# Kernel optimization log

Hardware: AMD Instinct MI355X
Metric: run time of the kernel (lower is better)

## Reference

```python
import jax, jax.numpy as jnp
import numpy as np

B, N, H, W = 1, 256, 32, 32
C_LIDAR, C_RGB, K, S = 64, 64, 16, 3
MLP3 = [128, 64, 64]


def _l2norm(x, eps=1e-12):
    n = jnp.linalg.norm(x, axis=-1, keepdims=True)
    return x / jnp.maximum(n, eps)


def _cal_sim(src, dst):
    # src [B,N,C], dst [B,M,C] -> [B,N,M,2] (cosine sim normalized two ways)
    s = _l2norm(src)
    d = _l2norm(dst)
    sim = jnp.einsum('bmc,bnc->bmn', d, s)  # [B,M,N]
    dst_src = sim / (jnp.max(sim, axis=2, keepdims=True) + 1e-10)
    src_dst = jnp.swapaxes(sim, 1, 2)       # [B,N,M]
    src_dst = src_dst / (jnp.max(src_dst, axis=2, keepdims=True) + 1e-6)
    return jnp.stack([src_dst, jnp.swapaxes(dst_src, 1, 2)], axis=-1)


def _mlp(x, layers):
    # 1x1 conv + (identity-init BN folded) + ReLU chain, channel-last
    for w, b in layers:
        x = jax.nn.relu(x @ w + b)
    return x


def _unfold(x, s):
    # F.unfold with zero pad s//2: [B,C,H,W] -> [B, H*W, s*s, C]
    p = s // 2
    b, c, h, w = x.shape
    xp = jnp.pad(x, ((0, 0), (0, 0), (p, p), (p, p)))
    pats = jnp.stack([xp[:, :, i:i + h, j:j + w] for i in range(s) for j in range(s)], axis=2)
    return pats.reshape(b, c, s * s, h * w).transpose(0, 3, 2, 1)


def _weighted_pnp(src_xyz, uv, wgt):
    # weighted SVD (Kabsch) head: lift uv to 3D at source depth, solve R,t
    z = src_xyz[..., 2:3]
    dst = jnp.concatenate([uv, jnp.ones_like(z)], axis=-1) * z
    wn = wgt / (jnp.sum(wgt, axis=-1, keepdims=True) + 1e-8)
    sc = jnp.einsum('bn,bnc->bc', wn, src_xyz)
    dc = jnp.einsum('bn,bnc->bc', wn, dst)
    s_c = src_xyz - sc[:, None]
    d_c = dst - dc[:, None]
    Hm = jnp.einsum('bn,bni,bnj->bij', wn, s_c, d_c)
    U, _, Vt = jnp.linalg.svd(Hm)
    V = jnp.swapaxes(Vt, -1, -2)
    det = jnp.linalg.det(jnp.einsum('bik,bjk->bij', V, U))
    diag = jnp.stack([jnp.ones_like(det), jnp.ones_like(det), det], axis=-1)
    R = jnp.einsum('bik,bk,bjk->bij', V, diag, U)
    t = dc - jnp.einsum('bij,bj->bi', R, sc)
    return R, t


def reference(warped_xyz, warped_points, RF3, RF3_index, lidar_z,
              w2_0, b2_0, w2_1, b2_1, w2_2, b2_2,
              w3_0, b3_0, w3_1, b3_1, w3_2, b3_2,
              w1_0, b1_0, w1_1, b1_1, w1_2, b1_2,
              wm_0, bm_0, wm_1, bm_1, wm_2, bm_2):
    b, n, _ = warped_xyz.shape
    _, ci, h, w = RF3.shape
    m = h * w
    xyz = warped_xyz * lidar_z                       # [B,N,3]
    rf = RF3.transpose(0, 2, 3, 1).reshape(b, m, ci)   # [B,M,Ci]
    rfi = RF3_index.transpose(0, 2, 3, 1).reshape(b, m, 3)

    src_dst_sim = _cal_sim(warped_points, rf)        # [B,N,M,2]

    # kNN grouping of the point cloud onto itself
    d2 = jnp.sum((xyz[:, :, None, :] - xyz[:, None, :, :]) ** 2, axis=-1)
    _, idx = jax.lax.top_k(-d2, K)                   # [B,N,K]
    gather = jax.vmap(lambda pts, i: pts[i])
    pc_xyz_g = gather(xyz, idx)                      # [B,N,K,3]
    pc_pts_g = gather(warped_points, idx)            # [B,N,K,C]
    diff = pc_xyz_g - xyz[:, :, None, :]
    dn = jnp.linalg.norm(diff, axis=-1, keepdims=True)
    pc_nbr = jnp.concatenate([pc_pts_g, diff, dn], axis=-1)
    wts = _mlp(pc_nbr, [(w2_0, b2_0), (w2_1, b2_1), (w2_2, b2_2)])
    wts = jnp.max(wts, axis=-1, keepdims=True)
    wts = jax.nn.softmax(wts, axis=-2)
    pc_feats = jnp.sum(wts * pc_pts_g, axis=-2)      # [B,N,C]

    # image 3x3 neighbor grouping via unfold
    rf_nbr_idx = _unfold(RF3_index, S)               # [B,M,SS,3]
    rf_nbr_pts = _unfold(RF3, S)                     # [B,M,SS,Ci]
    iw = _mlp(jnp.concatenate([rf_nbr_idx, rf_nbr_pts], axis=-1),
              [(w3_0, b3_0), (w3_1, b3_1), (w3_2, b3_2)])
    iw = jnp.max(iw, axis=-1, keepdims=True)
    iw = jax.nn.softmax(iw, axis=-2)
    img_feats = jnp.sum(iw * rf_nbr_pts, axis=-2)    # [B,M,Ci]

    nbr_sim = _cal_sim(pc_feats, img_feats)          # [B,N,M,2]

    feats = jnp.concatenate([
        jnp.broadcast_to(xyz[:, :, None, :], (b, n, m, 3)),
        jnp.broadcast_to(rfi[:, None, :, :], (b, n, m, 3)),
        jnp.broadcast_to(warped_points[:, :, None, :], (b, n, m, warped_points.shape[-1])),
        jnp.broadcast_to(rf[:, None, :, :], (b, n, m, ci)),
        src_dst_sim, nbr_sim], axis=-1)              # [B,N,M,6+C+Ci+4]
    feats = _mlp(feats, [(w1_0, b1_0), (w1_1, b1_1), (w1_2, b1_2)])

    aw = jax.nn.softmax(jnp.max(feats, axis=-1), axis=-1)   # [B,N,M]
    corres_uv1 = jnp.einsum('bnm,bmc->bnc', aw, rfi)         # [B,N,3]
    att = jnp.einsum('bnm,bnmc->bnc', aw, feats)             # [B,N,64]
    att = _mlp(att, [(wm_0, bm_0), (wm_1, bm_1)])
    logits = att @ wm_2 + bm_2                               # [B,N,2]
    weights = jax.nn.softmax(logits, axis=-1)
    w_in = jnp.argmax(weights, axis=-1).astype(weights.dtype)
    R, t = _weighted_pnp(xyz, corres_uv1[..., :2], w_in)
    return R, t, weights


def setup_inputs():
    key = jax.random.key(0)
    ks = jax.random.split(key, 32)
    f32 = jnp.float32
    inp = {}
    inp['warped_xyz'] = jax.random.normal(ks[0], (B, N, 3), f32)
    inp['warped_points'] = jax.random.normal(ks[1], (B, N, C_LIDAR), f32)
    inp['RF3'] = jax.random.normal(ks[2], (B, C_RGB, H, W), f32)
    inp['RF3_index'] = jax.random.normal(ks[3], (B, 3, H, W), f32)
    inp['lidar_z'] = jax.random.uniform(ks[4], (B, N, 1), f32, 0.5, 2.0)
    wdims = {'w2_0': (4 + C_LIDAR, C_LIDAR), 'w2_1': (C_LIDAR, C_LIDAR), 'w2_2': (C_LIDAR, C_LIDAR),
             'w3_0': (3 + C_RGB, C_RGB), 'w3_1': (C_RGB, C_RGB), 'w3_2': (C_RGB, C_RGB),
             'w1_0': (6 + C_RGB + C_LIDAR + 4, MLP3[0]), 'w1_1': (MLP3[0], MLP3[1]), 'w1_2': (MLP3[1], MLP3[2]),
             'wm_0': (MLP3[2], MLP3[2]), 'wm_1': (MLP3[2], MLP3[0]), 'wm_2': (MLP3[0], 2)}
    for i, (name, d) in enumerate(wdims.items()):
        inp[name] = jax.random.normal(ks[5 + i], d, f32) * 0.05
        inp['b' + name[1:]] = jnp.zeros((d[1],), f32)
    return inp
```

## Files before the change

kernel.cpp:

```cpp
#include <hip/hip_runtime.h>
#include <math.h>


typedef _Float16 f16;
typedef __attribute__((ext_vector_type(4))) _Float16 f16x4;
typedef __attribute__((ext_vector_type(8))) _Float16 f16x8;
typedef __attribute__((ext_vector_type(4))) float f32x4;

constexpr int WS_XYZ  = 0;
constexpr int WS_RF   = 768;
constexpr int WS_RFI  = WS_RF   + 65536;
constexpr int WS_SN   = WS_RFI  + 3072;
constexpr int WS_DN   = WS_SN   + 16384;
constexpr int WS_SIM1 = WS_DN   + 65536;
constexpr int WS_RM1  = WS_SIM1 + 262144;
constexpr int WS_CM1  = WS_RM1  + 1024;
constexpr int WS_PCF  = WS_CM1  + 256;
constexpr int WS_IMGF = WS_PCF  + 16384;
constexpr int WS_PCN  = WS_IMGF + 65536;
constexpr int WS_IMGN = WS_PCN  + 16384;
constexpr int WS_SIM2 = WS_IMGN + 65536;
constexpr int WS_RM2  = WS_SIM2 + 262144;
constexpr int WS_CM2  = WS_RM2  + 1024;
constexpr int WS_B1   = WS_CM2  + 256;
constexpr int WS_B2   = WS_B1   + 32768;
constexpr int WS_ATT  = WS_B2   + 131072;
constexpr int WS_UV   = WS_ATT  + 16384;
constexpr int WS_WIN  = WS_UV   + 768;
constexpr int WS_KNN  = WS_WIN  + 256;
constexpr int WS_PM   = WS_KNN  + 4096;
constexpr int WS_PS   = WS_PM   + 2048;
constexpr int WS_PATT = WS_PS   + 2048;
constexpr int WS_PUV  = WS_PATT + 131072;
constexpr int WS_W11T = WS_PUV  + 6144;
constexpr int WS_W12T = WS_W11T + 4096;
constexpr int WS_G3   = WS_W12T + 2048;
constexpr int WS_SIMF = WS_G3   + 65600;

__global__ __launch_bounds__(256) void prep_kernel(float* ws, const float* wxyz,
                                                   const float* lz, const float* RF3,
                                                   const float* RFI, const float* w11,
                                                   const float* w12) {
    int i = blockIdx.x * 256 + threadIdx.x;
    if (i < 768) {
        int n = i / 3;
        ws[WS_XYZ + i] = wxyz[i] * lz[n];
    } else if (i < 768 + 65536) {
        int j = i - 768; int mm = j >> 6, c = j & 63;
        ws[WS_RF + j] = RF3[c * 1024 + mm];
    } else if (i < 768 + 65536 + 3072) {
        int j = i - (768 + 65536); int mm = j / 3, c = j - mm * 3;
        ws[WS_RFI + j] = RFI[c * 1024 + mm];
    } else if (i < 69376 + 8192) {
        int j = i - 69376; int col = j >> 7, k = j & 127;
        ((f16*)(ws + WS_W11T))[col * 128 + k] = (f16)w11[k * 64 + col];
    } else if (i < 69376 + 12288) {
        int j = i - (69376 + 8192); int col = j >> 6, k = j & 63;
        ((f16*)(ws + WS_W12T))[col * 64 + k] = (f16)w12[k * 64 + col];
    }
}

__global__ __launch_bounds__(64) void rownorm2_kernel(const float* sA, float* dA,
                                                      const float* sB, float* dB) {
    int b = blockIdx.x, t = threadIdx.x;
    const float* src; float* dst; int r;
    if (b < 256) { src = sA; dst = dA; r = b; }
    else         { src = sB; dst = dB; r = b - 256; }
    float v = src[r * 64 + t];
    float s = v * v;
    for (int o = 32; o > 0; o >>= 1) s += __shfl_down(s, o);
    s = __shfl(s, 0);
    float nrm = sqrtf(s);
    dst[r * 64 + t] = v / fmaxf(nrm, 1e-12f);
}

__global__ __launch_bounds__(256) void sim_kernel(const float* dn, const float* sn,
                                                  float* sim, float* rmax) {
    __shared__ __align__(16) float dv[64];
    __shared__ float red[256];
    int m = blockIdx.x, t = threadIdx.x;
    if (t < 64) dv[t] = dn[m * 64 + t];
    __syncthreads();
    float acc = 0.f;
    const float4* sp = (const float4*)(sn + t * 64);
    const float4* dp = (const float4*)dv;
    for (int i = 0; i < 16; i++) {
        float4 s4 = sp[i], d4 = dp[i];
        acc += s4.x * d4.x + s4.y * d4.y + s4.z * d4.z + s4.w * d4.w;
    }
    sim[m * 256 + t] = acc;
    red[t] = acc; __syncthreads();
    for (int s = 128; s > 0; s >>= 1) {
        if (t < s) red[t] = fmaxf(red[t], red[t + s]);
        __syncthreads();
    }
    if (t == 0) rmax[m] = red[0];
}

__global__ __launch_bounds__(256) void simfeat_kernel(float* ws) {
    __shared__ float red[256];
    int n = blockIdx.x, t = threadIdx.x;
    const float* sim1 = ws + WS_SIM1;  const float* rm1g = ws + WS_RM1;
    const float* sim2 = ws + WS_SIM2;  const float* rm2g = ws + WS_RM2;
    f16* simfg = (f16*)(ws + WS_SIMF);
    float s1v[4], s2v[4];
    float mx1 = -INFINITY, mx2 = -INFINITY;
    for (int j = 0; j < 4; j++) {
        int m = t + j * 256;
        s1v[j] = sim1[m * 256 + n]; mx1 = fmaxf(mx1, s1v[j]);
        s2v[j] = sim2[m * 256 + n]; mx2 = fmaxf(mx2, s2v[j]);
    }
    red[t] = mx1; __syncthreads();
    for (int s = 128; s > 0; s >>= 1) {
        if (t < s) red[t] = fmaxf(red[t], red[t + s]);
        __syncthreads();
    }
    float cm1 = red[0];
    __syncthreads();
    red[t] = mx2; __syncthreads();
    for (int s = 128; s > 0; s >>= 1) {
        if (t < s) red[t] = fmaxf(red[t], red[t + s]);
        __syncthreads();
    }
    float cm2 = red[0];
    for (int j = 0; j < 4; j++) {
        int m = t + j * 256;
        float r1 = rm1g[m], r2 = rm2g[m];
        float f0 = s1v[j] / (cm1 + 1e-6f);
        float f1 = s1v[j] / (r1 + 1e-10f);
        float f2 = s2v[j] / (cm2 + 1e-6f);
        float f3 = s2v[j] / (r2 + 1e-10f);
        *(f16x4*)&simfg[(n * 1024 + m) * 4] =
            (f16x4){(f16)f0, (f16)f1, (f16)f2, (f16)f3};
    }
}

__global__ __launch_bounds__(256) void knn_kernel(float* ws) {
    const float* xyz = ws + WS_XYZ;
    int* knn = (int*)(ws + WS_KNN);
    __shared__ float px[256], py[256], pz[256], d2[256];
    __shared__ float rv[256];
    __shared__ int   ri[256];
    int n = blockIdx.x, t = threadIdx.x;
    px[t] = xyz[t * 3 + 0]; py[t] = xyz[t * 3 + 1]; pz[t] = xyz[t * 3 + 2];
    __syncthreads();
    float dx = px[t] - px[n], dy = py[t] - py[n], dz = pz[t] - pz[n];
    d2[t] = dx * dx + dy * dy + dz * dz;
    __syncthreads();
    for (int k = 0; k < 16; k++) {
        rv[t] = d2[t]; ri[t] = t;
        __syncthreads();
        for (int s = 128; s > 0; s >>= 1) {
            if (t < s) {
                float v2 = rv[t + s]; int i2 = ri[t + s];
                if (v2 < rv[t] || (v2 == rv[t] && i2 < ri[t])) { rv[t] = v2; ri[t] = i2; }
            }
            __syncthreads();
        }
        if (t == 0) { knn[n * 16 + k] = ri[0]; d2[ri[0]] = INFINITY; }
        __syncthreads();
    }
}

__global__ __launch_bounds__(256) void mlp2_kernel(float* ws, const float* wpts,
        const float* w0, const float* b0, const float* w1, const float* b1,
        const float* w2, const float* b2) {
    __shared__ float x[16 * 68], hA[16 * 68], hB[16 * 68];
    __shared__ int   kn[16];
    __shared__ float wv[16], wts[16];
    int n = blockIdx.x, t = threadIdx.x;
    const float* xyz = ws + WS_XYZ;
    const int* knn = (const int*)(ws + WS_KNN);
    if (t < 16) kn[t] = knn[n * 16 + t];
    __syncthreads();
    for (int i = t; i < 1024; i += 256) {
        int k = i >> 6, c = i & 63;
        x[k * 68 + c] = wpts[kn[k] * 64 + c];
    }
    if (t < 16) {
        int i = kn[t];
        float dx = xyz[i * 3 + 0] - xyz[n * 3 + 0];
        float dy = xyz[i * 3 + 1] - xyz[n * 3 + 1];
        float dz = xyz[i * 3 + 2] - xyz[n * 3 + 2];
        x[t * 68 + 64] = dx; x[t * 68 + 65] = dy; x[t * 68 + 66] = dz;
        x[t * 68 + 67] = sqrtf(dx * dx + dy * dy + dz * dz);
    }
    __syncthreads();
    for (int o = t; o < 1024; o += 256) {
        int k = o >> 6, j = o & 63; float acc = b0[j];
        for (int i = 0; i < 68; i++) acc += x[k * 68 + i] * w0[i * 64 + j];
        hA[k * 68 + j] = fmaxf(acc, 0.f);
    }
    __syncthreads();
    for (int o = t; o < 1024; o += 256) {
        int k = o >> 6, j = o & 63; float acc = b1[j];
        for (int i = 0; i < 64; i++) acc += hA[k * 68 + i] * w1[i * 64 + j];
        hB[k * 68 + j] = fmaxf(acc, 0.f);
    }
    __syncthreads();
    for (int o = t; o < 1024; o += 256) {
        int k = o >> 6, j = o & 63; float acc = b2[j];
        for (int i = 0; i < 64; i++) acc += hB[k * 68 + i] * w2[i * 64 + j];
        hA[k * 68 + j] = fmaxf(acc, 0.f);
    }
    __syncthreads();
    if (t < 16) {
        float mx = -INFINITY;
        for (int j = 0; j < 64; j++) mx = fmaxf(mx, hA[t * 68 + j]);
        wv[t] = mx;
    }
    __syncthreads();
    if (t < 16) {
        float mx = -INFINITY;
        for (int k = 0; k < 16; k++) mx = fmaxf(mx, wv[k]);
        float sum = 0.f;
        for (int k = 0; k < 16; k++) sum += expf(wv[k] - mx);
        wts[t] = expf(wv[t] - mx) / sum;
    }
    __syncthreads();
    if (t < 64) {
        float acc = 0.f;
        for (int k = 0; k < 16; k++) acc += wts[k] * x[k * 68 + t];
        ws[WS_PCF + n * 64 + t] = acc;
    }
}

__global__ __launch_bounds__(64) void g3_kernel(float* ws, const float* w0, const float* b0) {
    int m = blockIdx.x, j = threadIdx.x;
    float acc = b0[j];
    if (m < 1024) {
        for (int i = 0; i < 3; i++)  acc += ws[WS_RFI + m * 3 + i] * w0[i * 64 + j];
        for (int c = 0; c < 64; c++) acc += ws[WS_RF + m * 64 + c] * w0[(3 + c) * 64 + j];
    }
    ws[WS_G3 + m * 64 + j] = fmaxf(acc, 0.f);
}

__global__ __launch_bounds__(256) void mlp3_kernel(float* ws,
        const float* w1, const float* b1, const float* w2, const float* b2) {
    __shared__ float x1[36 * 68], h2[36 * 68];
    __shared__ float h3v[36], iw9[36];
    int m0 = blockIdx.x * 4, t = threadIdx.x;
    const float* G = ws + WS_G3;
    const float* rf = ws + WS_RF;
    for (int i = t; i < 36 * 64; i += 256) {
        int row = i >> 6, c = i & 63;
        int mi = row / 9, kk = row - mi * 9;
        int m = m0 + mi; int y = m >> 5, x = m & 31;
        int dy = kk / 3 - 1, dx = kk % 3 - 1;
        int ny = y + dy, nx = x + dx;
        bool val = (ny >= 0 && ny < 32 && nx >= 0 && nx < 32);
        int idx = val ? (ny * 32 + nx) : 1024;
        x1[row * 68 + c] = G[idx * 64 + c];
    }
    __syncthreads();
    for (int o = t; o < 36 * 64; o += 256) {
        int row = o >> 6, c = o & 63; float acc = b1[c];
        for (int i = 0; i < 64; i++) acc += x1[row * 68 + i] * w1[i * 64 + c];
        h2[row * 68 + c] = fmaxf(acc, 0.f);
    }
    __syncthreads();
    for (int o = t; o < 36 * 64; o += 256) {
        int row = o >> 6, c = o & 63; float acc = b2[c];
        for (int i = 0; i < 64; i++) acc += h2[row * 68 + i] * w2[i * 64 + c];
        x1[row * 68 + c] = fmaxf(acc, 0.f);
    }
    __syncthreads();
    if (t < 36) {
        float mx = -INFINITY;
        for (int c = 0; c < 64; c++) mx = fmaxf(mx, x1[t * 68 + c]);
        h3v[t] = mx;
    }
    __syncthreads();
    if (t < 36) {
        int mi = t / 9;
        float mx = -INFINITY;
        for (int k = 0; k < 9; k++) mx = fmaxf(mx, h3v[mi * 9 + k]);
        float sum = 0.f;
        for (int k = 0; k < 9; k++) sum += expf(h3v[mi * 9 + k] - mx);
        iw9[t] = expf(h3v[t] - mx) / sum;
    }
    __syncthreads();
    {
        int mi = t >> 6, c = t & 63;
        int m = m0 + mi; int y = m >> 5, x = m & 31;
        float acc = 0.f;
        for (int kk = 0; kk < 9; kk++) {
            int dy = kk / 3 - 1, dx = kk % 3 - 1;
            int ny = y + dy, nx = x + dx;
            bool val = (ny >= 0 && ny < 32 && nx >= 0 && nx < 32);
            if (val) acc += iw9[mi * 9 + kk] * rf[(ny * 32 + nx) * 64 + c];
        }
        ws[WS_IMGF + m * 64 + c] = acc;
    }
}

__global__ __launch_bounds__(128) void base12_kernel(float* ws, const float* wpts,
                                                     const float* w10, const float* b10) {
    int b = blockIdx.x, j = threadIdx.x;
    if (b < 256) {
        int n = b;
        float acc = b10[j];
        for (int i = 0; i < 3; i++)  acc += ws[WS_XYZ + n * 3 + i] * w10[i * 128 + j];
        for (int c = 0; c < 64; c++) acc += wpts[n * 64 + c] * w10[(6 + c) * 128 + j];
        ws[WS_B1 + n * 128 + j] = acc;
    } else {
        int m = b - 256;
        float acc = 0.f;
        for (int i = 0; i < 3; i++)  acc += ws[WS_RFI + m * 3 + i] * w10[(3 + i) * 128 + j];
        for (int c = 0; c < 64; c++) acc += ws[WS_RF + m * 64 + c] * w10[(70 + c) * 128 + j];
        ws[WS_B2 + m * 128 + j] = acc;
    }
}

__global__ __launch_bounds__(256) void mlp1_kernel(float* ws, const float* w10,
        const float* b11, const float* b12) {
    __shared__ __align__(16) f16 H1h[64 * 136];
    __shared__ __align__(16) f16 H2h[64 * 72];
    __shared__ float base1n[128];
    __shared__ float simw[4 * 128];
    __shared__ float rmPart[4][64];
    int n = blockIdx.y, seg = blockIdx.x, t = threadIdx.x;
    int wave = t >> 6, lane = t & 63, q = lane >> 4, l16 = lane & 15;
    int col = wave * 16 + l16;
    const float* base2 = ws + WS_B2;
    const float* rfig = ws + WS_RFI;
    const f16* simfg = (const f16*)(ws + WS_SIMF);
    const f16* w11t = (const f16*)(ws + WS_W11T);
    const f16* w12t = (const f16*)(ws + WS_W12T);
    if (t < 128) base1n[t] = ws[WS_B1 + n * 128 + t];
    for (int i = t; i < 512; i += 256) simw[i] = w10[134 * 128 + i];
    f16x8 B2f[4], B3f[2];
    for (int s = 0; s < 4; s++) B2f[s] = *(const f16x8*)&w11t[col * 128 + s * 32 + q * 8];
    for (int s = 0; s < 2; s++) B3f[s] = *(const f16x8*)&w12t[col * 64 + s * 32 + q * 8];
    float bias2 = b11[col], bias3 = b12[col];
    float attAcc = 0.f;
    float uv0 = 0.f, uv1 = 0.f, uv2 = 0.f;
    float Mv = -INFINITY, Sv = 0.f;
    int mBeg = seg * 128;
    __syncthreads();
    for (int c4 = 0; c4 < 2; c4++) {
        int m0 = mBeg + c4 * 64;
        for (int idx = t; idx < 2048; idx += 256) {
            int row = idx >> 5, k4 = (idx & 31) * 4;
            int m = m0 + row;
            f16x4 sf = *(const f16x4*)&simfg[(n * 1024 + m) * 4];
            float s0 = (float)sf[0], s1 = (float)sf[1], s2 = (float)sf[2], s3 = (float)sf[3];
            float4 bs = *(const float4*)&base2[m * 128 + k4];
            float4 b1v = *(const float4*)&base1n[k4];
            float4 w0v = *(const float4*)&simw[k4];
            float4 w1v = *(const float4*)&simw[128 + k4];
            float4 w2v = *(const float4*)&simw[256 + k4];
            float4 w3v = *(const float4*)&simw[384 + k4];
            float v0 = b1v.x + bs.x + s0 * w0v.x + s1 * w1v.x + s2 * w2v.x + s3 * w3v.x;
            float v1 = b1v.y + bs.y + s0 * w0v.y + s1 * w1v.y + s2 * w2v.y + s3 * w3v.y;
            float v2 = b1v.z + bs.z + s0 * w0v.z + s1 * w1v.z + s2 * w2v.z + s3 * w3v.z;
            float v3 = b1v.w + bs.w + s0 * w0v.w + s1 * w1v.w + s2 * w2v.w + s3 * w3v.w;
            *(f16x4*)&H1h[row * 136 + k4] = (f16x4){
                (f16)fmaxf(v0, 0.f), (f16)fmaxf(v1, 0.f),
                (f16)fmaxf(v2, 0.f), (f16)fmaxf(v3, 0.f)};
        }
        __syncthreads();
        f32x4 a[4];
        for (int tl = 0; tl < 4; tl++) a[tl] = (f32x4){bias2, bias2, bias2, bias2};
        for (int s = 0; s < 4; s++)
            for (int tl = 0; tl < 4; tl++) {
                f16x8 f = *(const f16x8*)&H1h[(tl * 16 + l16) * 136 + s * 32 + q * 8];
                a[tl] = __builtin_amdgcn_mfma_f32_16x16x32_f16(f, B2f[s], a[tl], 0, 0, 0);
            }
        for (int tl = 0; tl < 4; tl++)
            for (int r = 0; r < 4; r++)
                H2h[(tl * 16 + q * 4 + r) * 72 + col] = (f16)fmaxf(a[tl][r], 0.f);
        __syncthreads();
        f32x4 c3[4];
        for (int tl = 0; tl < 4; tl++) c3[tl] = (f32x4){bias3, bias3, bias3, bias3};
        for (int s = 0; s < 2; s++)
            for (int tl = 0; tl < 4; tl++) {
                f16x8 f = *(const f16x8*)&H2h[(tl * 16 + l16) * 72 + s * 32 + q * 8];
                c3[tl] = __builtin_amdgcn_mfma_f32_16x16x32_f16(f, B3f[s], c3[tl], 0, 0, 0);
            }
        for (int tl = 0; tl < 4; tl++)
            for (int r = 0; r < 4; r++)
                c3[tl][r] = fmaxf(c3[tl][r], 0.f);
        for (int tl = 0; tl < 4; tl++)
            for (int r = 0; r < 4; r++) {
                float v = c3[tl][r];
                v = fmaxf(v, __shfl_xor(v, 1));
                v = fmaxf(v, __shfl_xor(v, 2));
                v = fmaxf(v, __shfl_xor(v, 4));
                v = fmaxf(v, __shfl_xor(v, 8));
                if (l16 == 0) rmPart[wave][tl * 16 + q * 4 + r] = v;
            }
        __syncthreads();
        float rmv = fmaxf(fmaxf(rmPart[0][lane], rmPart[1][lane]),
// ... 102 lines not shown
        const int PQ[3][2] = {{0, 1}, {0, 2}, {1, 2}};
        for (int pp = 0; pp < 3; pp++) {
            int p = PQ[pp][0], q = PQ[pp][1];
            double apq = A[p][q];
            if (fabs(apq) < 1e-300) continue;
            double tau = (A[q][q] - A[p][p]) / (2.0 * apq);
            double tt = (tau >= 0.0 ? 1.0 : -1.0) / (fabs(tau) + sqrt(1.0 + tau * tau));
            double c = 1.0 / sqrt(1.0 + tt * tt), s = tt * c;
            for (int k = 0; k < 3; k++) {
                double akp = A[k][p], akq = A[k][q];
                A[k][p] = c * akp - s * akq; A[k][q] = s * akp + c * akq;
            }
            for (int k = 0; k < 3; k++) {
                double apk = A[p][k], aqk = A[q][k];
                A[p][k] = c * apk - s * aqk; A[q][k] = s * apk + c * aqk;
            }
            for (int k = 0; k < 3; k++) {
                double vkp = V[k][p], vkq = V[k][q];
                V[k][p] = c * vkp - s * vkq; V[k][q] = s * vkp + c * vkq;
            }
        }
    }
    double lam[3] = {A[0][0], A[1][1], A[2][2]};
    int o0 = 0, o1 = 1, o2 = 2;
    if (lam[o0] < lam[o1]) { int tp = o0; o0 = o1; o1 = tp; }
    if (lam[o0] < lam[o2]) { int tp = o0; o0 = o2; o2 = tp; }
    if (lam[o1] < lam[o2]) { int tp = o1; o1 = o2; o2 = tp; }
    int ord[3] = {o0, o1, o2};
    double v[3][3], u[3][3], R[3][3];
    for (int k = 0; k < 3; k++)
        for (int i = 0; i < 3; i++) v[k][i] = V[i][ord[k]];
    double sv0 = sqrt(fmax(lam[o0], 0.0));
    if (!(sv0 > 1e-150)) {
        for (int i = 0; i < 3; i++)
            for (int j = 0; j < 3; j++) R[i][j] = (i == j) ? 1.0 : 0.0;
    } else {
        double nn[3];
        for (int k = 0; k < 3; k++) {
            for (int i = 0; i < 3; i++)
                u[k][i] = Hd[i][0] * v[k][0] + Hd[i][1] * v[k][1] + Hd[i][2] * v[k][2];
            nn[k] = sqrt(u[k][0] * u[k][0] + u[k][1] * u[k][1] + u[k][2] * u[k][2]);
        }
        for (int i = 0; i < 3; i++) u[0][i] /= nn[0];
        if (nn[1] > 1e-12 * nn[0]) {
            for (int i = 0; i < 3; i++) u[1][i] /= nn[1];
        } else {
            int e = (fabs(u[0][0]) <= fabs(u[0][1]) && fabs(u[0][0]) <= fabs(u[0][2])) ? 0
                    : ((fabs(u[0][1]) <= fabs(u[0][2])) ? 1 : 2);
            double ev[3] = {0, 0, 0}; ev[e] = 1.0;
            double d0 = ev[0] * u[0][0] + ev[1] * u[0][1] + ev[2] * u[0][2];
            double w1v[3], wn2 = 0;
            for (int i = 0; i < 3; i++) { w1v[i] = ev[i] - d0 * u[0][i]; wn2 += w1v[i] * w1v[i]; }
            wn2 = sqrt(wn2);
            for (int i = 0; i < 3; i++) u[1][i] = w1v[i] / wn2;
        }
        if (nn[2] > 1e-10 * nn[0]) {
            for (int i = 0; i < 3; i++) u[2][i] /= nn[2];
        } else {
            u[2][0] = u[0][1] * u[1][2] - u[0][2] * u[1][1];
            u[2][1] = u[0][2] * u[1][0] - u[0][0] * u[1][2];
            u[2][2] = u[0][0] * u[1][1] - u[0][1] * u[1][0];
        }
        double cr[3] = {u[1][1] * u[2][2] - u[1][2] * u[2][1],
                        u[1][2] * u[2][0] - u[1][0] * u[2][2],
                        u[1][0] * u[2][1] - u[1][1] * u[2][0]};
        double detU = u[0][0] * cr[0] + u[0][1] * cr[1] + u[0][2] * cr[2];
        double cv[3] = {v[1][1] * v[2][2] - v[1][2] * v[2][1],
                        v[1][2] * v[2][0] - v[1][0] * v[2][2],
                        v[1][0] * v[2][1] - v[1][1] * v[2][0]};
        double detV = v[0][0] * cv[0] + v[0][1] * cv[1] + v[0][2] * cv[2];
        double dsign = detU * detV;
        for (int i = 0; i < 3; i++)
            for (int j = 0; j < 3; j++)
                R[i][j] = v[0][i] * u[0][j] + v[1][i] * u[1][j] + dsign * v[2][i] * u[2][j];
    }
    for (int i = 0; i < 3; i++) {
        double ti = dc[i] - (R[i][0] * sc[0] + R[i][1] * sc[1] + R[i][2] * sc[2]);
        out[9 + i] = (float)ti;
        for (int j = 0; j < 3; j++) out[i * 3 + j] = (float)R[i][j];
    }
}

__global__ __launch_bounds__(256) void pnp_kernel(float* ws, float* out) {
    __shared__ double red[256];
    int t = threadIdx.x;
    double w = (double)ws[WS_WIN + t];
    double x0 = ws[WS_XYZ + t * 3 + 0];
    double x1 = ws[WS_XYZ + t * 3 + 1];
    double x2 = ws[WS_XYZ + t * 3 + 2];
    double z = x2;
    double dd0 = (double)ws[WS_UV + t * 3 + 0] * z;
    double dd1 = (double)ws[WS_UV + t * 3 + 1] * z;
    double dd2 = z;
    auto reduce = [&](double v) -> double {
        red[t] = v; __syncthreads();
        for (int s = 128; s > 0; s >>= 1) {
            if (t < s) red[t] += red[t + s];
            __syncthreads();
        }
        double r = red[0]; __syncthreads();
        return r;
    };
    double wsum = reduce(w);
    double sx0 = reduce(w * x0), sx1 = reduce(w * x1), sx2 = reduce(w * x2);
    double sd0 = reduce(w * dd0), sd1 = reduce(w * dd1), sd2 = reduce(w * dd2);
    double inv = 1.0 / (wsum + 1e-8);
    double sc[3] = {sx0 * inv, sx1 * inv, sx2 * inv};
    double dc[3] = {sd0 * inv, sd1 * inv, sd2 * inv};
    double wn = w * inv;
    double a0 = x0 - sc[0], a1 = x1 - sc[1], a2 = x2 - sc[2];
    double b0 = dd0 - dc[0], b1 = dd1 - dc[1], b2 = dd2 - dc[2];
    double Hm[9];
    Hm[0] = reduce(wn * a0 * b0); Hm[1] = reduce(wn * a0 * b1); Hm[2] = reduce(wn * a0 * b2);
    Hm[3] = reduce(wn * a1 * b0); Hm[4] = reduce(wn * a1 * b1); Hm[5] = reduce(wn * a1 * b2);
    Hm[6] = reduce(wn * a2 * b0); Hm[7] = reduce(wn * a2 * b1); Hm[8] = reduce(wn * a2 * b2);
    if (t == 0) compute_rt(Hm, sc, dc, out);
}

extern "C" void kernel_launch(void* const* d_in, const int* in_sizes, int n_in,
                              void* d_out, int out_size, void* d_ws, size_t ws_size,
                              hipStream_t stream) {
    float* ws = (float*)d_ws;
    const float* wxyz = (const float*)d_in[0];
    const float* wpts = (const float*)d_in[1];
    const float* RF3  = (const float*)d_in[2];
    const float* RFI  = (const float*)d_in[3];
    const float* lz   = (const float*)d_in[4];
    const float* w2_0 = (const float*)d_in[5];  const float* b2_0 = (const float*)d_in[6];
    const float* w2_1 = (const float*)d_in[7];  const float* b2_1 = (const float*)d_in[8];
    const float* w2_2 = (const float*)d_in[9];  const float* b2_2 = (const float*)d_in[10];
    const float* w3_0 = (const float*)d_in[11]; const float* b3_0 = (const float*)d_in[12];
    const float* w3_1 = (const float*)d_in[13]; const float* b3_1 = (const float*)d_in[14];
    const float* w3_2 = (const float*)d_in[15]; const float* b3_2 = (const float*)d_in[16];
    const float* w1_0 = (const float*)d_in[17]; const float* b1_0 = (const float*)d_in[18];
    const float* w1_1 = (const float*)d_in[19]; const float* b1_1 = (const float*)d_in[20];
    const float* w1_2 = (const float*)d_in[21]; const float* b1_2 = (const float*)d_in[22];
    const float* wm_0 = (const float*)d_in[23]; const float* bm_0 = (const float*)d_in[24];
    const float* wm_1 = (const float*)d_in[25]; const float* bm_1 = (const float*)d_in[26];
    const float* wm_2 = (const float*)d_in[27]; const float* bm_2 = (const float*)d_in[28];
    float* out = (float*)d_out;

    prep_kernel<<<319, 256, 0, stream>>>(ws, wxyz, lz, RF3, RFI, w1_1, w1_2);
    rownorm2_kernel<<<1280, 64, 0, stream>>>(wpts, ws + WS_SN, ws + WS_RF, ws + WS_DN);
    sim_kernel<<<1024, 256, 0, stream>>>(ws + WS_DN, ws + WS_SN, ws + WS_SIM1, ws + WS_RM1);
    knn_kernel<<<256, 256, 0, stream>>>(ws);
    mlp2_kernel<<<256, 256, 0, stream>>>(ws, wpts, w2_0, b2_0, w2_1, b2_1, w2_2, b2_2);
    g3_kernel<<<1025, 64, 0, stream>>>(ws, w3_0, b3_0);
    mlp3_kernel<<<256, 256, 0, stream>>>(ws, w3_1, b3_1, w3_2, b3_2);
    rownorm2_kernel<<<1280, 64, 0, stream>>>(ws + WS_PCF, ws + WS_PCN, ws + WS_IMGF, ws + WS_IMGN);
    sim_kernel<<<1024, 256, 0, stream>>>(ws + WS_IMGN, ws + WS_PCN, ws + WS_SIM2, ws + WS_RM2);
    simfeat_kernel<<<256, 256, 0, stream>>>(ws);
    base12_kernel<<<1280, 128, 0, stream>>>(ws, wpts, w1_0, b1_0);
    mlp1_kernel<<<dim3(8, 256), 256, 0, stream>>>(ws, w1_0, b1_1, b1_2);
    combinehead_kernel<<<256, 128, 0, stream>>>(ws, wm_0, bm_0, wm_1, bm_1, wm_2, bm_2, out);
    pnp_kernel<<<1, 256, 0, stream>>>(ws, out);
}
```

Before: 262.8 us.

## Fuse pipeline stages to cut kernel launches and fold normalization into producers

Reduces the launch count from 14 to 9 kernels. Independent stages (g3, base12 and knn; mlp2 and mlp3) are merged into multi-role kernels selected by block index. The row L2 normalization is folded into sim1 as reciprocal-norm scaling and into the mlp2/mlp3 epilogues, which removes the rownorm passes. Max reductions now use wave shuffles, and the pnp reductions are batched so fewer barrier rounds run. The risks are block-role divergence and higher shared memory per block in the merged kernels.

```diff
diff --git a/kernel.cpp b/kernel.cpp
--- a/kernel.cpp
+++ b/kernel.cpp
@@ -11,6 +11,8 @@
 constexpr int WS_RF   = 768;
 constexpr int WS_RFI  = WS_RF   + 65536;
 constexpr int WS_SN   = WS_RFI  + 3072;
+constexpr int WS_RS   = WS_SN;
+constexpr int WS_RD   = WS_SN   + 256;
 constexpr int WS_DN   = WS_SN   + 16384;
 constexpr int WS_SIM1 = WS_DN   + 65536;
 constexpr int WS_RM1  = WS_SIM1 + 262144;
@@ -40,61 +42,85 @@
 __global__ __launch_bounds__(256) void prep_kernel(float* ws, const float* wxyz,
                                                    const float* lz, const float* RF3,
                                                    const float* RFI, const float* w11,
-                                                   const float* w12) {
-    int i = blockIdx.x * 256 + threadIdx.x;
-    if (i < 768) {
-        int n = i / 3;
-        ws[WS_XYZ + i] = wxyz[i] * lz[n];
-    } else if (i < 768 + 65536) {
-        int j = i - 768; int mm = j >> 6, c = j & 63;
-        ws[WS_RF + j] = RF3[c * 1024 + mm];
-    } else if (i < 768 + 65536 + 3072) {
-        int j = i - (768 + 65536); int mm = j / 3, c = j - mm * 3;
-        ws[WS_RFI + j] = RFI[c * 1024 + mm];
-    } else if (i < 69376 + 8192) {
-        int j = i - 69376; int col = j >> 7, k = j & 127;
-        ((f16*)(ws + WS_W11T))[col * 128 + k] = (f16)w11[k * 64 + col];
-    } else if (i < 69376 + 12288) {
-        int j = i - (69376 + 8192); int col = j >> 6, k = j & 63;
-        ((f16*)(ws + WS_W12T))[col * 64 + k] = (f16)w12[k * 64 + col];
-    }
-}
-
-__global__ __launch_bounds__(64) void rownorm2_kernel(const float* sA, float* dA,
-                                                      const float* sB, float* dB) {
-    int b = blockIdx.x, t = threadIdx.x;
-    const float* src; float* dst; int r;
-    if (b < 256) { src = sA; dst = dA; r = b; }
-    else         { src = sB; dst = dB; r = b - 256; }
-    float v = src[r * 64 + t];
-    float s = v * v;
-    for (int o = 32; o > 0; o >>= 1) s += __shfl_down(s, o);
-    s = __shfl(s, 0);
-    float nrm = sqrtf(s);
-    dst[r * 64 + t] = v / fmaxf(nrm, 1e-12f);
-}
-
-__global__ __launch_bounds__(256) void sim_kernel(const float* dn, const float* sn,
-                                                  float* sim, float* rmax) {
+                                                   const float* w12, const float* wpts) {
+    int b = blockIdx.x;
+    if (b < 319) {
+        int i = b * 256 + threadIdx.x;
+        if (i < 768) {
+            int n = i / 3;
+            ws[WS_XYZ + i] = wxyz[i] * lz[n];
+        } else if (i < 768 + 65536) {
+            int j = i - 768; int mm = j >> 6, c = j & 63;
+            ws[WS_RF + j] = RF3[c * 1024 + mm];
+        } else if (i < 768 + 65536 + 3072) {
+            int j = i - (768 + 65536); int mm = j / 3, c = j - mm * 3;
+            ws[WS_RFI + j] = RFI[c * 1024 + mm];
+        } else if (i < 69376 + 8192) {
+            int j = i - 69376; int col = j >> 7, k = j & 127;
+            ((f16*)(ws + WS_W11T))[col * 128 + k] = (f16)w11[k * 64 + col];
+        } else if (i < 69376 + 12288) {
+            int j = i - (69376 + 8192); int col = j >> 6, k = j & 63;
+            ((f16*)(ws + WS_W12T))[col * 64 + k] = (f16)w12[k * 64 + col];
+        }
+    } else if (b == 319) {
+        int n = threadIdx.x;
+        float s = 0.f;
+        for (int c = 0; c < 64; c++) { float v = wpts[n * 64 + c]; s += v * v; }
+        ws[WS_RS + n] = 1.f / fmaxf(sqrtf(s), 1e-12f);
+    } else {
+        int m = (b - 320) * 256 + threadIdx.x;
+        float s = 0.f;
+        for (int c = 0; c < 64; c++) { float v = RF3[c * 1024 + m]; s += v * v; }
+        ws[WS_RD + m] = 1.f / fmaxf(sqrtf(s), 1e-12f);
+    }
+}
+
+__global__ __launch_bounds__(256) void sim1s_kernel(float* ws, const float* wpts) {
     __shared__ __align__(16) float dv[64];
-    __shared__ float red[256];
+    __shared__ float wred[4];
     int m = blockIdx.x, t = threadIdx.x;
-    if (t < 64) dv[t] = dn[m * 64 + t];
+    int wave = t >> 6, lane = t & 63;
+    const float* rf = ws + WS_RF;
+    if (t < 64) dv[t] = rf[m * 64 + t];
     __syncthreads();
     float acc = 0.f;
-    const float4* sp = (const float4*)(sn + t * 64);
+    const float4* sp = (const float4*)(wpts + t * 64);
     const float4* dp = (const float4*)dv;
     for (int i = 0; i < 16; i++) {
         float4 s4 = sp[i], d4 = dp[i];
         acc += s4.x * d4.x + s4.y * d4.y + s4.z * d4.z + s4.w * d4.w;
     }
-    sim[m * 256 + t] = acc;
-    red[t] = acc; __syncthreads();
-    for (int s = 128; s > 0; s >>= 1) {
-        if (t < s) red[t] = fmaxf(red[t], red[t + s]);
-        __syncthreads();
-    }
-    if (t == 0) rmax[m] = red[0];
+    acc = acc * ws[WS_RD + m] * ws[WS_RS + t];
+    ws[WS_SIM1 + m * 256 + t] = acc;
+    float mx = acc;
+    for (int o = 32; o > 0; o >>= 1) mx = fmaxf(mx, __shfl_down(mx, o));
+    if (lane == 0) wred[wave] = mx;
+    __syncthreads();
+    if (t == 0)
+        ws[WS_RM1 + m] = fmaxf(fmaxf(wred[0], wred[1]), fmaxf(wred[2], wred[3]));
+}
+
+__global__ __launch_bounds__(256) void sim2_kernel(float* ws) {
+    __shared__ __align__(16) float dv[64];
+    __shared__ float wred[4];
+    int m = blockIdx.x, t = threadIdx.x;
+    int wave = t >> 6, lane = t & 63;
+    if (t < 64) dv[t] = ws[WS_IMGN + m * 64 + t];
+    __syncthreads();
+    float acc = 0.f;
+    const float4* sp = (const float4*)(ws + WS_PCN + t * 64);
+    const float4* dp = (const float4*)dv;
+    for (int i = 0; i < 16; i++) {
+        float4 s4 = sp[i], d4 = dp[i];
+        acc += s4.x * d4.x + s4.y * d4.y + s4.z * d4.z + s4.w * d4.w;
+    }
+    ws[WS_SIM2 + m * 256 + t] = acc;
+    float mx = acc;
+    for (int o = 32; o > 0; o >>= 1) mx = fmaxf(mx, __shfl_down(mx, o));
+    if (lane == 0) wred[wave] = mx;
+    __syncthreads();
+    if (t == 0)
+        ws[WS_RM2 + m] = fmaxf(fmaxf(wred[0], wred[1]), fmaxf(wred[2], wred[3]));
 }
 
 __global__ __launch_bounds__(256) void simfeat_kernel(float* ws) {
@@ -135,180 +161,192 @@
     }
 }
 
-__global__ __launch_bounds__(256) void knn_kernel(float* ws) {
-    const float* xyz = ws + WS_XYZ;
-    int* knn = (int*)(ws + WS_KNN);
+__global__ __launch_bounds__(256) void mid_kernel(float* ws, const float* wpts,
+        const float* w30, const float* b30, const float* w10, const float* b10) {
+    int b = blockIdx.x, t = threadIdx.x;
     __shared__ float px[256], py[256], pz[256], d2[256];
     __shared__ float rv[256];
     __shared__ int   ri[256];
-    int n = blockIdx.x, t = threadIdx.x;
-    px[t] = xyz[t * 3 + 0]; py[t] = xyz[t * 3 + 1]; pz[t] = xyz[t * 3 + 2];
-    __syncthreads();
-    float dx = px[t] - px[n], dy = py[t] - py[n], dz = pz[t] - pz[n];
-    d2[t] = dx * dx + dy * dy + dz * dz;
-    __syncthreads();
-    for (int k = 0; k < 16; k++) {
-        rv[t] = d2[t]; ri[t] = t;
-        __syncthreads();
-        for (int s = 128; s > 0; s >>= 1) {
-            if (t < s) {
-                float v2 = rv[t + s]; int i2 = ri[t + s];
-                if (v2 < rv[t] || (v2 == rv[t] && i2 < ri[t])) { rv[t] = v2; ri[t] = i2; }
-            }
+    if (b < 257) {
+        int m = b * 4 + (t >> 6), j = t & 63;
+        if (m < 1025) {
+            float acc = b30[j];
+            if (m < 1024) {
+                for (int i = 0; i < 3; i++)  acc += ws[WS_RFI + m * 3 + i] * w30[i * 64 + j];
+                for (int c = 0; c < 64; c++) acc += ws[WS_RF + m * 64 + c] * w30[(3 + c) * 64 + j];
+            }
+            ws[WS_G3 + m * 64 + j] = fmaxf(acc, 0.f);
+        }
+    } else if (b < 897) {
+        int bb = (b - 257) * 2 + (t >> 7);
+        int j = t & 127;
+        if (bb < 256) {
+            int n = bb;
+            float acc = b10[j];
+            for (int i = 0; i < 3; i++)  acc += ws[WS_XYZ + n * 3 + i] * w10[i * 128 + j];
+            for (int c = 0; c < 64; c++) acc += wpts[n * 64 + c] * w10[(6 + c) * 128 + j];
+            ws[WS_B1 + n * 128 + j] = acc;
+        } else {
+            int m = bb - 256;
+            float acc = 0.f;
+            for (int i = 0; i < 3; i++)  acc += ws[WS_RFI + m * 3 + i] * w10[(3 + i) * 128 + j];
+            for (int c = 0; c < 64; c++) acc += ws[WS_RF + m * 64 + c] * w10[(70 + c) * 128 + j];
+            ws[WS_B2 + m * 128 + j] = acc;
+        }
+    } else {
+        const float* xyz = ws + WS_XYZ;
+        int* knn = (int*)(ws + WS_KNN);
+        int n = b - 897;
+        px[t] = xyz[t * 3 + 0]; py[t] = xyz[t * 3 + 1]; pz[t] = xyz[t * 3 + 2];
+        __syncthreads();
+        float dx = px[t] - px[n], dy = py[t] - py[n], dz = pz[t] - pz[n];
+        d2[t] = dx * dx + dy * dy + dz * dz;
+        __syncthreads();
+        for (int k = 0; k < 16; k++) {
+            rv[t] = d2[t]; ri[t] = t;
             __syncthreads();
-        }
-        if (t == 0) { knn[n * 16 + k] = ri[0]; d2[ri[0]] = INFINITY; }
-        __syncthreads();
-    }
-}
-
-__global__ __launch_bounds__(256) void mlp2_kernel(float* ws, const float* wpts,
-        const float* w0, const float* b0, const float* w1, const float* b1,
-        const float* w2, const float* b2) {
-    __shared__ float x[16 * 68], hA[16 * 68], hB[16 * 68];
+            for (int s = 128; s > 0; s >>= 1) {
+                if (t < s) {
+                    float v2 = rv[t + s]; int i2 = ri[t + s];
+                    if (v2 < rv[t] || (v2 == rv[t] && i2 < ri[t])) { rv[t] = v2; ri[t] = i2; }
+                }
+                __syncthreads();
+            }
+            if (t == 0) { knn[n * 16 + k] = ri[0]; d2[ri[0]] = INFINITY; }
+            __syncthreads();
+        }
+    }
+}
+
+__global__ __launch_bounds__(256) void mlp23_kernel(float* ws, const float* wpts,
+        const float* w20, const float* b20, const float* w21, const float* b21,
+        const float* w22, const float* b22,
+        const float* w31, const float* b31, const float* w32, const float* b32) {
+    __shared__ float sbuf[36 * 68 * 2];
+    __shared__ float small1[36], small2[36];
     __shared__ int   kn[16];
-    __shared__ float wv[16], wts[16];
-    int n = blockIdx.x, t = threadIdx.x;
-    const float* xyz = ws + WS_XYZ;
-    const int* knn = (const int*)(ws + WS_KNN);
-    if (t < 16) kn[t] = knn[n * 16 + t];
-    __syncthreads();
-    for (int i = t; i < 1024; i += 256) {
-        int k = i >> 6, c = i & 63;
-        x[k * 68 + c] = wpts[kn[k] * 64 + c];
-    }
-    if (t < 16) {
-        int i = kn[t];
-        float dx = xyz[i * 3 + 0] - xyz[n * 3 + 0];
-        float dy = xyz[i * 3 + 1] - xyz[n * 3 + 1];
-        float dz = xyz[i * 3 + 2] - xyz[n * 3 + 2];
-        x[t * 68 + 64] = dx; x[t * 68 + 65] = dy; x[t * 68 + 66] = dz;
-        x[t * 68 + 67] = sqrtf(dx * dx + dy * dy + dz * dz);
-    }
-    __syncthreads();
-    for (int o = t; o < 1024; o += 256) {
-        int k = o >> 6, j = o & 63; float acc = b0[j];
-        for (int i = 0; i < 68; i++) acc += x[k * 68 + i] * w0[i * 64 + j];
-        hA[k * 68 + j] = fmaxf(acc, 0.f);
-    }
-    __syncthreads();
-    for (int o = t; o < 1024; o += 256) {
-        int k = o >> 6, j = o & 63; float acc = b1[j];
-        for (int i = 0; i < 64; i++) acc += hA[k * 68 + i] * w1[i * 64 + j];
-        hB[k * 68 + j] = fmaxf(acc, 0.f);
-    }
-    __syncthreads();
-    for (int o = t; o < 1024; o += 256) {
-        int k = o >> 6, j = o & 63; float acc = b2[j];
-        for (int i = 0; i < 64; i++) acc += hB[k * 68 + i] * w2[i * 64 + j];
-        hA[k * 68 + j] = fmaxf(acc, 0.f);
-    }
-    __syncthreads();
-    if (t < 16) {
-        float mx = -INFINITY;
-        for (int j = 0; j < 64; j++) mx = fmaxf(mx, hA[t * 68 + j]);
-        wv[t] = mx;
-    }
-    __syncthreads();
-    if (t < 16) {
-        float mx = -INFINITY;
-        for (int k = 0; k < 16; k++) mx = fmaxf(mx, wv[k]);
-        float sum = 0.f;
-        for (int k = 0; k < 16; k++) sum += expf(wv[k] - mx);
-        wts[t] = expf(wv[t] - mx) / sum;
-    }
-    __syncthreads();
-    if (t < 64) {
-        float acc = 0.f;
-        for (int k = 0; k < 16; k++) acc += wts[k] * x[k * 68 + t];
-        ws[WS_PCF + n * 64 + t] = acc;
-    }
-}
-
-__global__ __launch_bounds__(64) void g3_kernel(float* ws, const float* w0, const float* b0) {
-    int m = blockIdx.x, j = threadIdx.x;
-    float acc = b0[j];
-    if (m < 1024) {
-        for (int i = 0; i < 3; i++)  acc += ws[WS_RFI + m * 3 + i] * w0[i * 64 + j];
-        for (int c = 0; c < 64; c++) acc += ws[WS_RF + m * 64 + c] * w0[(3 + c) * 64 + j];
-    }
-    ws[WS_G3 + m * 64 + j] = fmaxf(acc, 0.f);
-}
-
-__global__ __launch_bounds__(256) void mlp3_kernel(float* ws,
-        const float* w1, const float* b1, const float* w2, const float* b2) {
-    __shared__ float x1[36 * 68], h2[36 * 68];
-    __shared__ float h3v[36], iw9[36];
-    int m0 = blockIdx.x * 4, t = threadIdx.x;
-    const float* G = ws + WS_G3;
-    const float* rf = ws + WS_RF;
-    for (int i = t; i < 36 * 64; i += 256) {
-        int row = i >> 6, c = i & 63;
-        int mi = row / 9, kk = row - mi * 9;
-        int m = m0 + mi; int y = m >> 5, x = m & 31;
-        int dy = kk / 3 - 1, dx = kk % 3 - 1;
-        int ny = y + dy, nx = x + dx;
-        bool val = (ny >= 0 && ny < 32 && nx >= 0 && nx < 32);
-        int idx = val ? (ny * 32 + nx) : 1024;
-        x1[row * 68 + c] = G[idx * 64 + c];
-    }
-    __syncthreads();
-    for (int o = t; o < 36 * 64; o += 256) {
-        int row = o >> 6, c = o & 63; float acc = b1[c];
-        for (int i = 0; i < 64; i++) acc += x1[row * 68 + i] * w1[i * 64 + c];
-        h2[row * 68 + c] = fmaxf(acc, 0.f);
-    }
-    __syncthreads();
-    for (int o = t; o < 36 * 64; o += 256) {
-        int row = o >> 6, c = o & 63; float acc = b2[c];
-        for (int i = 0; i < 64; i++) acc += h2[row * 68 + i] * w2[i * 64 + c];
-        x1[row * 68 + c] = fmaxf(acc, 0.f);
-    }
-    __syncthreads();
-    if (t < 36) {
-        float mx = -INFINITY;
-        for (int c = 0; c < 64; c++) mx = fmaxf(mx, x1[t * 68 + c]);
-        h3v[t] = mx;
-    }
-    __syncthreads();
-    if (t < 36) {
-        int mi = t / 9;
-        float mx = -INFINITY;
-        for (int k = 0; k < 9; k++) mx = fmaxf(mx, h3v[mi * 9 + k]);
-        float sum = 0.f;
-        for (int k = 0; k < 9; k++) sum += expf(h3v[mi * 9 + k] - mx);
-        iw9[t] = expf(h3v[t] - mx) / sum;
-    }
-    __syncthreads();
-    {
-        int mi = t >> 6, c = t & 63;
-        int m = m0 + mi; int y = m >> 5, x = m & 31;
-        float acc = 0.f;
-        for (int kk = 0; kk < 9; kk++) {
+    int b = blockIdx.x, t = threadIdx.x;
+    if (b < 256) {
+        int n = b;
+        float* x  = sbuf;
+        float* hA = sbuf + 1088;
+        float* hB = sbuf + 2176;
+        const float* xyz = ws + WS_XYZ;
+        const int* knn = (const int*)(ws + WS_KNN);
+        if (t < 16) kn[t] = knn[n * 16 + t];
+        __syncthreads();
+        for (int i = t; i < 1024; i += 256) {
+            int k = i >> 6, c = i & 63;
+            x[k * 68 + c] = wpts[kn[k] * 64 + c];
+        }
+        if (t < 16) {
+            int i = kn[t];
+            float dx = xyz[i * 3 + 0] - xyz[n * 3 + 0];
+            float dy = xyz[i * 3 + 1] - xyz[n * 3 + 1];
+            float dz = xyz[i * 3 + 2] - xyz[n * 3 + 2];
+            x[t * 68 + 64] = dx; x[t * 68 + 65] = dy; x[t * 68 + 66] = dz;
+            x[t * 68 + 67] = sqrtf(dx * dx + dy * dy + dz * dz);
+        }
+        __syncthreads();
+        for (int o = t; o < 1024; o += 256) {
+            int k = o >> 6, j = o & 63; float acc = b20[j];
+            for (int i = 0; i < 68; i++) acc += x[k * 68 + i] * w20[i * 64 + j];
+            hA[k * 68 + j] = fmaxf(acc, 0.f);
+        }
+        __syncthreads();
+        for (int o = t; o < 1024; o += 256) {
+            int k = o >> 6, j = o & 63; float acc = b21[j];
+            for (int i = 0; i < 64; i++) acc += hA[k * 68 + i] * w21[i * 64 + j];
+            hB[k * 68 + j] = fmaxf(acc, 0.f);
+        }
+        __syncthreads();
+        for (int o = t; o < 1024; o += 256) {
+            int k = o >> 6, j = o & 63; float acc = b22[j];
+            for (int i = 0; i < 64; i++) acc += hB[k * 68 + i] * w22[i * 64 + j];
+            hA[k * 68 + j] = fmaxf(acc, 0.f);
+        }
+        __syncthreads();
+        if (t < 16) {
+            float mx = -INFINITY;
+            for (int j = 0; j < 64; j++) mx = fmaxf(mx, hA[t * 68 + j]);
+            small1[t] = mx;
+        }
+        __syncthreads();
+        if (t < 16) {
+            float mx = -INFINITY;
+            for (int k = 0; k < 16; k++) mx = fmaxf(mx, small1[k]);
+            float sum = 0.f;
+            for (int k = 0; k < 16; k++) sum += expf(small1[k] - mx);
+            small2[t] = expf(small1[t] - mx) / sum;
+        }
+        __syncthreads();
+        if (t < 64) {
+            float acc = 0.f;
+            for (int k = 0; k < 16; k++) acc += small2[k] * x[k * 68 + t];
+            float s = acc * acc;
+            for (int o = 32; o > 0; o >>= 1) s += __shfl_down(s, o);
+            s = __shfl(s, 0);
+            ws[WS_PCN + n * 64 + t] = acc / fmaxf(sqrtf(s), 1e-12f);
+        }
+    } else {
+        int m0 = (b - 256) * 4;
+        float* x1 = sbuf;
+        float* h2 = sbuf + 2448;
+        const float* G = ws + WS_G3;
+        const float* rf = ws + WS_RF;
+        for (int i = t; i < 36 * 64; i += 256) {
+            int row = i >> 6, c = i & 63;
+            int mi = row / 9, kk = row - mi * 9;
+            int m = m0 + mi; int y = m >> 5, x = m & 31;
             int dy = kk / 3 - 1, dx = kk % 3 - 1;
             int ny = y + dy, nx = x + dx;
             bool val = (ny >= 0 && ny < 32 && nx >= 0 && nx < 32);
-            if (val) acc += iw9[mi * 9 + kk] * rf[(ny * 32 + nx) * 64 + c];
-        }
-        ws[WS_IMGF + m * 64 + c] = acc;
-    }
-}
-
-__global__ __launch_bounds__(128) void base12_kernel(float* ws, const float* wpts,
-                                                     const float* w10, const float* b10) {
-    int b = blockIdx.x, j = threadIdx.x;
-    if (b < 256) {
-        int n = b;
-        float acc = b10[j];
-        for (int i = 0; i < 3; i++)  acc += ws[WS_XYZ + n * 3 + i] * w10[i * 128 + j];
-        for (int c = 0; c < 64; c++) acc += wpts[n * 64 + c] * w10[(6 + c) * 128 + j];
-        ws[WS_B1 + n * 128 + j] = acc;
-    } else {
-        int m = b - 256;
-        float acc = 0.f;
-        for (int i = 0; i < 3; i++)  acc += ws[WS_RFI + m * 3 + i] * w10[(3 + i) * 128 + j];
-        for (int c = 0; c < 64; c++) acc += ws[WS_RF + m * 64 + c] * w10[(70 + c) * 128 + j];
-        ws[WS_B2 + m * 128 + j] = acc;
+            int idx = val ? (ny * 32 + nx) : 1024;
+            x1[row * 68 + c] = G[idx * 64 + c];
+        }
+        __syncthreads();
+        for (int o = t; o < 36 * 64; o += 256) {
+            int row = o >> 6, c = o & 63; float acc = b31[c];
+            for (int i = 0; i < 64; i++) acc += x1[row * 68 + i] * w31[i * 64 + c];
+            h2[row * 68 + c] = fmaxf(acc, 0.f);
+        }
+        __syncthreads();
+        for (int o = t; o < 36 * 64; o += 256) {
+            int row = o >> 6, c = o & 63; float acc = b32[c];
+            for (int i = 0; i < 64; i++) acc += h2[row * 68 + i] * w32[i * 64 + c];
+            x1[row * 68 + c] = fmaxf(acc, 0.f);
+        }
+        __syncthreads();
+        if (t < 36) {
+            float mx = -INFINITY;
+            for (int c = 0; c < 64; c++) mx = fmaxf(mx, x1[t * 68 + c]);
+            small1[t] = mx;
+        }
+        __syncthreads();
+        if (t < 36) {
+            int mi = t / 9;
+            float mx = -INFINITY;
+            for (int k = 0; k < 9; k++) mx = fmaxf(mx, small1[mi * 9 + k]);
+            float sum = 0.f;
+            for (int k = 0; k < 9; k++) sum += expf(small1[mi * 9 + k] - mx);
+            small2[t] = expf(small1[t] - mx) / sum;
+        }
+        __syncthreads();
+        {
+            int mi = t >> 6, c = t & 63;
+            int m = m0 + mi; int y = m >> 5, x = m & 31;
+            float acc = 0.f;
+            for (int kk = 0; kk < 9; kk++) {
+                int dy = kk / 3 - 1, dx = kk % 3 - 1;
+                int ny = y + dy, nx = x + dx;
+                bool val = (ny >= 0 && ny < 32 && nx >= 0 && nx < 32);
+                if (val) acc += small2[mi * 9 + kk] * rf[(ny * 32 + nx) * 64 + c];
+            }
+            float s = acc * acc;
+            for (int o = 32; o > 0; o >>= 1) s += __shfl_down(s, o);
+            s = __shfl(s, 0);
+            ws[WS_IMGN + m * 64 + c] = acc / fmaxf(sqrtf(s), 1e-12f);
+        }
     }
 }
 
@@ -577,7 +615,7 @@
 }
 
 __global__ __launch_bounds__(256) void pnp_kernel(float* ws, float* out) {
-    __shared__ double red[256];
+    __shared__ double red[9][256];
     int t = threadIdx.x;
     double w = (double)ws[WS_WIN + t];
     double x0 = ws[WS_XYZ + t * 3 + 0];
@@ -587,29 +625,39 @@
     double dd0 = (double)ws[WS_UV + t * 3 + 0] * z;
     double dd1 = (double)ws[WS_UV + t * 3 + 1] * z;
     double dd2 = z;
-    auto reduce = [&](double v) -> double {
-        red[t] = v; __syncthreads();
-        for (int s = 128; s > 0; s >>= 1) {
-            if (t < s) red[t] += red[t + s];
-            __syncthreads();
-        }
-        double r = red[0]; __syncthreads();
-        return r;
-    };
-    double wsum = reduce(w);
-    double sx0 = reduce(w * x0), sx1 = reduce(w * x1), sx2 = reduce(w * x2);
-    double sd0 = reduce(w * dd0), sd1 = reduce(w * dd1), sd2 = reduce(w * dd2);
+    red[0][t] = w;
+    red[1][t] = w * x0; red[2][t] = w * x1; red[3][t] = w * x2;
+    red[4][t] = w * dd0; red[5][t] = w * dd1; red[6][t] = w * dd2;
+    __syncthreads();
+    for (int s = 128; s > 0; s >>= 1) {
+        if (t < s)
+            for (int k = 0; k < 7; k++) red[k][t] += red[k][t + s];
+        __syncthreads();
+    }
+    double wsum = red[0][0];
+    double sx0 = red[1][0], sx1 = red[2][0], sx2 = red[3][0];
+    double sd0 = red[4][0], sd1 = red[5][0], sd2 = red[6][0];
+    __syncthreads();
     double inv = 1.0 / (wsum + 1e-8);
     double sc[3] = {sx0 * inv, sx1 * inv, sx2 * inv};
     double dc[3] = {sd0 * inv, sd1 * inv, sd2 * inv};
     double wn = w * inv;
     double a0 = x0 - sc[0], a1 = x1 - sc[1], a2 = x2 - sc[2];
     double b0 = dd0 - dc[0], b1 = dd1 - dc[1], b2 = dd2 - dc[2];
-    double Hm[9];
-    Hm[0] = reduce(wn * a0 * b0); Hm[1] = reduce(wn * a0 * b1); Hm[2] = reduce(wn * a0 * b2);
-    Hm[3] = reduce(wn * a1 * b0); Hm[4] = reduce(wn * a1 * b1); Hm[5] = reduce(wn * a1 * b2);
-    Hm[6] = reduce(wn * a2 * b0); Hm[7] = reduce(wn * a2 * b1); Hm[8] = reduce(wn * a2 * b2);
-    if (t == 0) compute_rt(Hm, sc, dc, out);
+    red[0][t] = wn * a0 * b0; red[1][t] = wn * a0 * b1; red[2][t] = wn * a0 * b2;
+    red[3][t] = wn * a1 * b0; red[4][t] = wn * a1 * b1; red[5][t] = wn * a1 * b2;
+    red[6][t] = wn * a2 * b0; red[7][t] = wn * a2 * b1; red[8][t] = wn * a2 * b2;
+    __syncthreads();
+    for (int s = 128; s > 0; s >>= 1) {
+        if (t < s)
+            for (int k = 0; k < 9; k++) red[k][t] += red[k][t + s];
+        __syncthreads();
+    }
+    if (t == 0) {
+        double Hm[9];
+        for (int k = 0; k < 9; k++) Hm[k] = red[k][0];
+        compute_rt(Hm, sc, dc, out);
+    }
 }
 
 extern "C" void kernel_launch(void* const* d_in, const int* in_sizes, int n_in,
@@ -635,17 +683,13 @@
     const float* wm_2 = (const float*)d_in[27]; const float* bm_2 = (const float*)d_in[28];
     float* out = (float*)d_out;
 
-    prep_kernel<<<319, 256, 0, stream>>>(ws, wxyz, lz, RF3, RFI, w1_1, w1_2);
-    rownorm2_kernel<<<1280, 64, 0, stream>>>(wpts, ws + WS_SN, ws + WS_RF, ws + WS_DN);
-    sim_kernel<<<1024, 256, 0, stream>>>(ws + WS_DN, ws + WS_SN, ws + WS_SIM1, ws + WS_RM1);
-    knn_kernel<<<256, 256, 0, stream>>>(ws);
-    mlp2_kernel<<<256, 256, 0, stream>>>(ws, wpts, w2_0, b2_0, w2_1, b2_1, w2_2, b2_2);
-    g3_kernel<<<1025, 64, 0, stream>>>(ws, w3_0, b3_0);
-    mlp3_kernel<<<256, 256, 0, stream>>>(ws, w3_1, b3_1, w3_2, b3_2);
-    rownorm2_kernel<<<1280, 64, 0, stream>>>(ws + WS_PCF, ws + WS_PCN, ws + WS_IMGF, ws + WS_IMGN);
-    sim_kernel<<<1024, 256, 0, stream>>>(ws + WS_IMGN, ws + WS_PCN, ws + WS_SIM2, ws + WS_RM2);
+    prep_kernel<<<324, 256, 0, stream>>>(ws, wxyz, lz, RF3, RFI, w1_1, w1_2, wpts);
+    sim1s_kernel<<<1024, 256, 0, stream>>>(ws, wpts);
+    mid_kernel<<<1153, 256, 0, stream>>>(ws, wpts, w3_0, b3_0, w1_0, b1_0);
+    mlp23_kernel<<<512, 256, 0, stream>>>(ws, wpts, w2_0, b2_0, w2_1, b2_1, w2_2, b2_2,
+                                          w3_1, b3_1, w3_2, b3_2);
+    sim2_kernel<<<1024, 256, 0, stream>>>(ws);
     simfeat_kernel<<<256, 256, 0, stream>>>(ws);
-    base12_kernel<<<1280, 128, 0, stream>>>(ws, wpts, w1_0, b1_0);
     mlp1_kernel<<<dim3(8, 256), 256, 0, stream>>>(ws, w1_0, b1_1, b1_2);
     combinehead_kernel<<<256, 128, 0, stream>>>(ws, wm_0, bm_0, wm_1, bm_1, wm_2, bm_2, out);
     pnp_kernel<<<1, 256, 0, stream>>>(ws, out);
```

New measurement: 235.8 us. 10.3% less time.
